# Kernel optimization log

Hardware: AMD Instinct MI355X
Metric: run time of the kernel (lower is better)

## Reference

```python
import jax, jax.numpy as jnp
import numpy as np

GROUPS = 32
EPS = 1e-5
N_HEADS = 4


def group_norm(x, w, b):
    # x: [B, C, T]; GroupNorm over (C/G, T) within each of G groups
    B, C, T = x.shape
    xg = x.reshape(B, GROUPS, (C // GROUPS) * T)
    mean = xg.mean(axis=-1, keepdims=True)
    var = xg.var(axis=-1, keepdims=True)
    xn = ((xg - mean) * jax.lax.rsqrt(var + EPS)).reshape(B, C, T)
    return xn * w[None, :, None] + b[None, :, None]


def setup_inputs() -> dict:
    key = jax.random.key(0)
    ks = jax.random.split(key, 5)
    B, C, H, W = 2, 256, 64, 64
    x = jax.random.normal(ks[0], (B, C, H, W), dtype=jnp.float32)
    norm_w = jnp.ones((C,), dtype=jnp.float32)
    norm_b = jnp.zeros((C,), dtype=jnp.float32)
    qkv_w = jax.random.normal(ks[1], (3 * C, C), dtype=jnp.float32) * (C ** -0.5)
    qkv_b = jax.random.normal(ks[2], (3 * C,), dtype=jnp.float32) * 0.02
    proj_w = jax.random.normal(ks[3], (C, C), dtype=jnp.float32) * (C ** -0.5)
    proj_b = jax.random.normal(ks[4], (C,), dtype=jnp.float32) * 0.02
    return {"x": x, "norm_w": norm_w, "norm_b": norm_b,
            "qkv_w": qkv_w, "qkv_b": qkv_b,
            "proj_w": proj_w, "proj_b": proj_b}


def reference(x, norm_w, norm_b, qkv_w, qkv_b, proj_w, proj_b):
    B, C, Hs, Ws = x.shape
    T = Hs * Ws
    xf = x.reshape(B, C, T)
    xn = group_norm(xf, norm_w, norm_b)
    # 1x1 conv1d == channel matmul: [3C,C] x [B,C,T] -> [B,3C,T]
    qkv = jnp.einsum('oc,bct->bot', qkv_w, xn) + qkv_b[None, :, None]
    ch = C // N_HEADS
    # legacy order: [B, H*3*ch, T] -> [B*H, 3*ch, T] -> split
    qkv_h = qkv.reshape(B * N_HEADS, 3 * ch, T)
    q, k, v = qkv_h[:, :ch], qkv_h[:, ch:2 * ch], qkv_h[:, 2 * ch:]
    scale = ch ** -0.25
    # full [B*H, T, T] score matrix, softmax in fp32 (faithful to source)
    weight = jnp.einsum('bct,bcs->bts', q * scale, k * scale)
    weight = jax.nn.softmax(weight.astype(jnp.float32), axis=-1).astype(qkv.dtype)
    a = jnp.einsum('bts,bcs->bct', weight, v).reshape(B, C, T)
    h = jnp.einsum('oc,bct->bot', proj_w, a) + proj_b[None, :, None]
    return (xf + h).reshape(B, C, Hs, Ws)
```

## Files before the change

### kernel.cpp

```cpp
#include <hip/hip_runtime.h>
#include <hip/hip_bf16.h>

#define B_    2
#define C_    256
#define T_    4096
#define GRP   32
#define CPG   8
#define NH    4
#define CH    64
#define K3C   768
#define SPLIT 4
#define GSL   8
#define NSTAT (B_ * GRP * GSL)
#define NCVT  128
#define LOG2E 1.4426950408889634f

typedef __attribute__((ext_vector_type(8))) short bf16x8;
typedef __attribute__((ext_vector_type(4))) float f32x4;
typedef __attribute__((ext_vector_type(16))) float f32x16;

#if __has_builtin(__builtin_amdgcn_exp2f)
#define EXP2(x) __builtin_amdgcn_exp2f(x)
#else
#define EXP2(x) exp2f(x)
#endif

__device__ __forceinline__ unsigned pk2(float a, float b) {
    __hip_bfloat162 h = __float22bfloat162_rn(make_float2(a, b));
    union { __hip_bfloat162 h2; unsigned u; } cv; cv.h2 = h;
    return cv.u;
}
__device__ __forceinline__ float bf2f(unsigned short u) {
    return __uint_as_float((unsigned)u << 16);
}

__device__ __forceinline__ void gl_lds16(const unsigned short* g, unsigned short* l) {
    __builtin_amdgcn_global_load_lds(
        (const __attribute__((address_space(1))) unsigned int*)g,
        (__attribute__((address_space(3))) unsigned int*)l,
        16, 0, 0);
}


__global__ __launch_bounds__(256) void pre_kernel(
    const float* __restrict__ x, float* __restrict__ stat,
    const float* __restrict__ qw, const float* __restrict__ pw,
    unsigned short* __restrict__ qwb, unsigned short* __restrict__ pwb) {
    int bid = blockIdx.x;
    int tid = threadIdx.x;
    if (bid < NSTAT) {
        int bg = bid >> 3, sl = bid & 7;
        const int SLN = CPG * T_ / GSL;
        const float* xp = x + (size_t)bg * CPG * T_ + (size_t)sl * SLN;
        float s = 0.f, s2 = 0.f;
        for (int i = tid * 4; i < SLN; i += 1024) {
            float4 v = *(const float4*)&xp[i];
            s  += (v.x + v.y) + (v.z + v.w);
            s2 += (v.x * v.x + v.y * v.y) + (v.z * v.z + v.w * v.w);
        }
        for (int off = 32; off > 0; off >>= 1) {
            s  += __shfl_down(s,  off);
            s2 += __shfl_down(s2, off);
        }
        __shared__ float rs[4], rs2[4];
        int wid = tid >> 6;
        if ((tid & 63) == 0) { rs[wid] = s; rs2[wid] = s2; }
        __syncthreads();
        if (tid == 0) {
            stat[bid * 2]     = (rs[0] + rs[1]) + (rs[2] + rs[3]);
            stat[bid * 2 + 1] = (rs2[0] + rs2[1]) + (rs2[2] + rs2[3]);
        }
    } else {
        int i = (bid - NSTAT) * 256 + tid;
        const int n1 = K3C * C_ / 8;
        const float* src; unsigned short* dst;
        if (i < n1) { src = qw + 8 * i; dst = qwb + 8 * i; }
        else { int j = i - n1; src = pw + 8 * j; dst = pwb + 8 * j; }
        float4 a = *(const float4*)src;
        float4 b = *(const float4*)(src + 4);
        uint4 u;
        u.x = pk2(a.x, a.y); u.y = pk2(a.z, a.w);
        u.z = pk2(b.x, b.y); u.w = pk2(b.z, b.w);
        *(uint4*)dst = u;
    }
}

__global__ __launch_bounds__(256) void gn_apply_kernel(
    const float* __restrict__ x, const float* __restrict__ stat,
    const float* __restrict__ w, const float* __restrict__ b,
    unsigned short* __restrict__ xnT) {
    int bg = blockIdx.x, sl = blockIdx.y;
    int batch = bg / GRP, g = bg % GRP;
    const float* xp = x + (size_t)bg * CPG * T_;
    int tid = threadIdx.x;

    float s = 0.f, s2 = 0.f;
#pragma unroll
    for (int i = 0; i < GSL; ++i) {
        s  += stat[(bg * GSL + i) * 2];
        s2 += stat[(bg * GSL + i) * 2 + 1];
    }
    float inv_n = 1.f / (float)(CPG * T_);
    float mean = s * inv_n;
    float var  = s2 * inv_n - mean * mean;
    float inv  = rsqrtf(var + 1e-5f);

    float wv[8], bv[8];
#pragma unroll
    for (int j = 0; j < 8; j++) {
        float ww = w[g * CPG + j] * inv;
        wv[j] = ww;
        bv[j] = b[g * CPG + j] - mean * ww;
    }
    int t0 = sl * (T_ / GSL);
#pragma unroll
    for (int rep = 0; rep < 2; ++rep) {
        int t = t0 + rep * 256 + tid;
        float v[8];
#pragma unroll
        for (int j = 0; j < 8; j++) v[j] = xp[(size_t)j * T_ + t] * wv[j] + bv[j];
        uint4 u;
        u.x = pk2(v[0], v[1]); u.y = pk2(v[2], v[3]);
        u.z = pk2(v[4], v[5]); u.w = pk2(v[6], v[7]);
        *(uint4*)&xnT[(((size_t)batch * 256 + (t >> 4)) * 32 + g) * 128
                      + (t & 15) * 8] = u;
    }
}

__global__ __launch_bounds__(256) void qkv_gemm_kernel(
    const unsigned short* __restrict__ Wb, const float* __restrict__ bias,
    const unsigned short* __restrict__ Xt, unsigned short* __restrict__ q_t,
    unsigned short* __restrict__ k_t, unsigned short* __restrict__ v_d) {
    int tb = blockIdx.x * 128;
    int by = blockIdx.y;
    int bz = blockIdx.z;
    int ob = by * 64;
    int tid = threadIdx.x;
    int l = tid & 15, oct = (tid >> 4) & 3, w = tid >> 6;

    __shared__ __align__(16) unsigned short SH[64 * 264];

#pragma unroll
    for (int j = 0; j < 8; ++j) {
        int idx = tid + 256 * j;
        int row = idx >> 5, ch = idx & 31;
        *(uint4*)&SH[row * 264 + ch * 8] =
            *(const uint4*)&Wb[(size_t)(ob + row) * C_ + ch * 8];
    }
    __syncthreads();

    f32x4 acc[4][2];
#pragma unroll
    for (int mf = 0; mf < 4; ++mf)
#pragma unroll
        for (int nf = 0; nf < 2; ++nf) acc[mf][nf] = (f32x4){0.f, 0.f, 0.f, 0.f};

#pragma unroll
    for (int kk = 0; kk < 8; ++kk) {
        int c0 = 32 * kk + 8 * oct;
        bf16x8 bfr[2];
#pragma unroll
        for (int nf = 0; nf < 2; ++nf)
            bfr[nf] = *(const bf16x8*)
                &Xt[(((size_t)bz * 256 + (tb >> 4) + 2 * w + nf) * 32
                     + 4 * kk + oct) * 128 + l * 8];
#pragma unroll
        for (int mf = 0; mf < 4; ++mf) {
            bf16x8 af = *(const bf16x8*)&SH[(16 * mf + l) * 264 + c0];
#pragma unroll
            for (int nf = 0; nf < 2; ++nf)
                acc[mf][nf] = __builtin_amdgcn_mfma_f32_16x16x32_bf16(af, bfr[nf], acc[mf][nf], 0, 0, 0);
        }
    }

    int head = by / 3, sec = by - 3 * head;
    int bh = bz * NH + head;

    if (sec < 2) {
        float scale = (sec == 0) ? 0.125f * LOG2E : 1.f;
        unsigned short* dst = ((sec == 0) ? q_t : k_t) + (size_t)bh * T_ * CH;
#pragma unroll
        for (int mf = 0; mf < 4; ++mf) {
            float bvs[4];
#pragma unroll
            for (int r = 0; r < 4; ++r) bvs[r] = bias[ob + 16 * mf + 4 * oct + r];
#pragma unroll
            for (int nf = 0; nf < 2; ++nf) {
                int t = tb + 32 * w + 16 * nf + l;
                float v0 = (acc[mf][nf][0] + bvs[0]) * scale;
                float v1 = (acc[mf][nf][1] + bvs[1]) * scale;
                float v2 = (acc[mf][nf][2] + bvs[2]) * scale;
                float v3 = (acc[mf][nf][3] + bvs[3]) * scale;
                uint2 u; u.x = pk2(v0, v1); u.y = pk2(v2, v3);
                *(uint2*)&dst[(size_t)t * CH + 16 * mf + 4 * oct] = u;
            }
        }
    } else {
        __syncthreads();
#pragma unroll
        for (int mf = 0; mf < 4; ++mf) {
            float bvs[4];
#pragma unroll
            for (int r = 0; r < 4; ++r) bvs[r] = bias[ob + 16 * mf + 4 * oct + r];
#pragma unroll
            for (int nf = 0; nf < 2; ++nf) {
                int tl = 32 * w + 16 * nf + l;
#pragma unroll
                for (int r = 0; r < 4; ++r) {
                    unsigned pv = pk2(acc[mf][nf][r] + bvs[r], 0.f);
                    SH[(16 * mf + 4 * oct + r) * 136 + tl] = (unsigned short)(pv & 0xffffu);
                }
            }
        }
        __syncthreads();
        unsigned short* vdst = v_d + (size_t)bh * CH * T_;
#pragma unroll
        for (int j = 0; j < 4; ++j) {
            int idx = tid + 256 * j;
            int row = idx >> 4, ch = idx & 15;
            *(uint4*)&vdst[(size_t)row * T_ + tb + ch * 8] =
                *(uint4*)&SH[row * 136 + ch * 8];
        }
    }
}

__global__ __launch_bounds__(256, 4) void attn_kernel(
    const unsigned short* __restrict__ q_t, const unsigned short* __restrict__ k_t,
    const unsigned short* __restrict__ v_d, unsigned short* __restrict__ Opart,
    float* __restrict__ lbuf) {
    int bh = blockIdx.y;
    int sp = blockIdx.z;
    int t0 = blockIdx.x * 128;
    int tid = threadIdx.x;
    int ln = tid & 63;
    int li = ln & 31;
    int hi = ln >> 5;
    int w  = tid >> 6;
    int l7 = li & 7;
    int sw = l7 ^ ((li >> 3) & 3);

    __shared__ __align__(16) unsigned short Kt[2][64 * 64];
    __shared__ __align__(16) unsigned short Vt[2][64 * 64];

    const unsigned short* qb = q_t + (size_t)bh * T_ * CH;
    const unsigned short* kb = k_t + (size_t)bh * T_ * CH;
    const unsigned short* vb = v_d + (size_t)bh * CH * T_;

    int tq = t0 + 32 * w + li;
    bf16x8 qf[4];
#pragma unroll
    for (int ks = 0; ks < 4; ++ks)
        qf[ks] = *(const bf16x8*)&qb[(size_t)tq * CH + ks * 16 + 8 * hi];

    int rsub = ln >> 3;
    int sch  = ln & 7;
    int cm8_0 = (sch ^ rsub ^ ((2 * w) & 3)) * 8;
    int cm8_1 = (sch ^ rsub ^ ((2 * w + 1) & 3)) * 8;
    int kr0 = 16 * w + rsub;

#define STAGE(buf, s0) do {                                                            \
    gl_lds16(kb + (size_t)((s0) + kr0) * CH + cm8_0,     &Kt[buf][(16 * w) * 64]);     \
    gl_lds16(kb + (size_t)((s0) + kr0 + 8) * CH + cm8_1, &Kt[buf][(16 * w + 8) * 64]); \
    gl_lds16(vb + (size_t)kr0 * T_ + (s0) + cm8_0,       &Vt[buf][(16 * w) * 64]);     \
    gl_lds16(vb + (size_t)(kr0 + 8) * T_ + (s0) + cm8_1, &Vt[buf][(16 * w + 8) * 64]); \
} while (0)

    f32x16 O0, O1;
#pragma unroll
    for (int i = 0; i < 16; ++i) { O0[i] = 0.f; O1[i] = 0.f; }
    float l_run = 0.f;

    int s_beg = sp * (T_ / SPLIT);
    const int NT = (T_ / SPLIT) / 64;

    STAGE(0, s_beg);
    __syncthreads();

    int cur = 0;
    for (int t = 0; t < NT; ++t) {
        if (t + 1 < NT) STAGE(cur ^ 1, s_beg + (t + 1) * 64);

        f32x16 S0, S1;
#pragma unroll
        for (int i = 0; i < 16; ++i) { S0[i] = 0.f; S1[i] = 0.f; }
        __builtin_amdgcn_s_setprio(1);
#pragma unroll
        for (int ks = 0; ks < 4; ++ks) {
            bf16x8 ka0 = *(const bf16x8*)
                &Kt[cur][li * 64 + (((2 * ks + hi) ^ sw) * 8)];
            bf16x8 ka1 = *(const bf16x8*)
                &Kt[cur][(32 + li) * 64 + (((2 * ks + hi) ^ sw) * 8)];
            S0 = __builtin_amdgcn_mfma_f32_32x32x16_bf16(ka0, qf[ks], S0, 0, 0, 0);
            S1 = __builtin_amdgcn_mfma_f32_32x32x16_bf16(ka1, qf[ks], S1, 0, 0, 0);
        }
        __builtin_amdgcn_s_setprio(0);

        unsigned W0[8], W1[8];
        float lloc = 0.f;
#pragma unroll
        for (int h = 0; h < 4; ++h) {
            float a0 = EXP2(S0[4 * h + 0]), a1 = EXP2(S0[4 * h + 1]);
            float a2 = EXP2(S0[4 * h + 2]), a3 = EXP2(S0[4 * h + 3]);
            float b0 = EXP2(S1[4 * h + 0]), b1 = EXP2(S1[4 * h + 1]);
            float b2 = EXP2(S1[4 * h + 2]), b3 = EXP2(S1[4 * h + 3]);
            lloc += ((a0 + a1) + (a2 + a3)) + ((b0 + b1) + (b2 + b3));
            W0[2 * h] = pk2(a0, a1); W0[2 * h + 1] = pk2(a2, a3);
            W1[2 * h] = pk2(b0, b1); W1[2 * h + 1] = pk2(b2, b3);
        }
        l_run += lloc;

        __builtin_amdgcn_s_setprio(1);
#pragma unroll
        for (int g = 0; g < 4; ++g) {
            int ks = g & 1;
            unsigned w0, w1, w2, w3;
            if (g < 2) {
                w0 = W0[4 * ks + 0]; w1 = W0[4 * ks + 1];
                w2 = W0[4 * ks + 2]; w3 = W0[4 * ks + 3];
            } else {
                w0 = W1[4 * ks + 0]; w1 = W1[4 * ks + 1];
                w2 = W1[4 * ks + 2]; w3 = W1[4 * ks + 3];
            }
            asm("v_permlane32_swap_b32 %0, %1" : "+v"(w0), "+v"(w2));
            asm("v_permlane32_swap_b32 %0, %1" : "+v"(w1), "+v"(w3));
            union { unsigned u[4]; bf16x8 v; } pu;
            pu.u[0] = w0; pu.u[1] = w1; pu.u[2] = w2; pu.u[3] = w3;
            bf16x8 va0 = *(const bf16x8*)
                &Vt[cur][li * 64 + (((2 * g + hi) ^ sw) * 8)];
            bf16x8 va1 = *(const bf16x8*)
                &Vt[cur][(32 + li) * 64 + (((2 * g + hi) ^ sw) * 8)];
            O0 = __builtin_amdgcn_mfma_f32_32x32x16_bf16(va0, pu.v, O0, 0, 0, 0);
            O1 = __builtin_amdgcn_mfma_f32_32x32x16_bf16(va1, pu.v, O1, 0, 0, 0);
        }
        __builtin_amdgcn_s_setprio(0);

        __syncthreads();
        cur ^= 1;
    }
#undef STAGE

    float lt = l_run + __shfl_xor(l_run, 32);
    float inv = 1.f / lt;
    size_t obase = ((size_t)(sp * 8 + bh) * 256 + (tq >> 4)) * 8;
    int ti = tq & 15;
#pragma unroll
    for (int cb = 0; cb < 2; ++cb) {
#pragma unroll
        for (int h = 0; h < 4; ++h) {
            float v0, v1, v2, v3;
            if (cb == 0) {
                v0 = O0[4 * h + 0]; v1 = O0[4 * h + 1];
                v2 = O0[4 * h + 2]; v3 = O0[4 * h + 3];
            } else {
                v0 = O1[4 * h + 0]; v1 = O1[4 * h + 1];
                v2 = O1[4 * h + 2]; v3 = O1[4 * h + 3];
            }
            uint2 u;
            u.x = pk2(v0 * inv, v1 * inv);
            u.y = pk2(v2 * inv, v3 * inv);
            *(uint2*)&Opart[(obase + 4 * cb + h) * 128 + ti * 8 + 4 * hi] = u;
        }
    }
    if (hi == 0) lbuf[(size_t)(sp * 8 + bh) * T_ + tq] = lt;
}

__global__ __launch_bounds__(256) void proj_gemm_kernel(
    const unsigned short* __restrict__ Wb, const float* __restrict__ bias,
    const unsigned short* __restrict__ Opart, const float* __restrict__ lbuf,
    const float* __restrict__ xres, float* __restrict__ out) {
    int tb = blockIdx.x * 64;
    int ob = blockIdx.y * 64;
    int bz = blockIdx.z;
    int tid = threadIdx.x;
    int l = tid & 15, oct = (tid >> 4) & 3, w = tid >> 6;

    __shared__ __align__(16) unsigned short SH[64 * 264];

#pragma unroll
    for (int j = 0; j < 8; ++j) {
        int idx = tid + 256 * j;
        int row = idx >> 5, ch = idx & 31;
        *(uint4*)&SH[row * 264 + ch * 8] =
            *(const uint4*)&Wb[(size_t)(ob + row) * C_ + ch * 8];
    }
    __syncthreads();

    int t = tb + 16 * w + l;

    float lwn[SPLIT][NH];
#pragma unroll
    for (int h = 0; h < NH; ++h) {
        float lw[SPLIT], lsum = 0.f;
#pragma unroll
        for (int sp = 0; sp < SPLIT; ++sp) {
            lw[sp] = lbuf[(size_t)(sp * 8 + bz * NH + h) * T_ + t];
            lsum += lw[sp];
        }
        float inv = 1.f / lsum;
#pragma unroll
        for (int sp = 0; sp < SPLIT; ++sp) lwn[sp][h] = lw[sp] * inv;
    }

    f32x4 acc[4];
#pragma unroll
    for (int mf = 0; mf < 4; ++mf) acc[mf] = (f32x4){0.f, 0.f, 0.f, 0.f};

#pragma unroll
    for (int kk = 0; kk < 8; ++kk) {
        int c0 = 32 * kk + 8 * oct;
        int h  = kk >> 1;
        int cc = 4 * (kk & 1) + oct;

        float o[8];
#pragma unroll
        for (int j = 0; j < 8; ++j) o[j] = 0.f;
#pragma unroll
        for (int sp = 0; sp < SPLIT; ++sp) {
            const unsigned short* p = Opart +
                (((size_t)(sp * 8 + bz * NH + h) * 256 + (t >> 4)) * 8 + cc) * 128
                + (t & 15) * 8;
            uint4 u = *(const uint4*)p;
            float s = lwn[sp][h];
            o[0] += bf2f((unsigned short)(u.x & 0xffffu)) * s;
            o[1] += bf2f((unsigned short)(u.x >> 16)) * s;
            o[2] += bf2f((unsigned short)(u.y & 0xffffu)) * s;
            o[3] += bf2f((unsigned short)(u.y >> 16)) * s;
            o[4] += bf2f((unsigned short)(u.z & 0xffffu)) * s;
            o[5] += bf2f((unsigned short)(u.z >> 16)) * s;
            o[6] += bf2f((unsigned short)(u.w & 0xffffu)) * s;
            o[7] += bf2f((unsigned short)(u.w >> 16)) * s;
        }
        union { uint4 u; bf16x8 v; } pb;
        pb.u.x = pk2(o[0], o[1]); pb.u.y = pk2(o[2], o[3]);
        pb.u.z = pk2(o[4], o[5]); pb.u.w = pk2(o[6], o[7]);

#pragma unroll
        for (int mf = 0; mf < 4; ++mf) {
            bf16x8 af = *(const bf16x8*)&SH[(16 * mf + l) * 264 + c0];
            acc[mf] = __builtin_amdgcn_mfma_f32_16x16x32_bf16(af, pb.v, acc[mf], 0, 0, 0);
        }
    }

#pragma unroll
    for (int mf = 0; mf < 4; ++mf) {
#pragma unroll
        for (int r = 0; r < 4; ++r) {
            int o = ob + 16 * mf + 4 * oct + r;
            size_t idx = ((size_t)bz * C_ + o) * T_ + t;
            out[idx] = acc[mf][r] + bias[o] + xres[idx];
        }
    }
}

extern "C" void kernel_launch(void* const* d_in, const int* in_sizes, int n_in,
                              void* d_out, int out_size, void* d_ws, size_t ws_size,
                              hipStream_t stream) {
    const float* x      = (const float*)d_in[0];
    const float* norm_w = (const float*)d_in[1];
    const float* norm_b = (const float*)d_in[2];
    const float* qkv_w  = (const float*)d_in[3];
    const float* qkv_b  = (const float*)d_in[4];
    const float* proj_w = (const float*)d_in[5];
    const float* proj_b = (const float*)d_in[6];
    float* out = (float*)d_out;

    char* p = (char*)d_ws;
    unsigned short* xnT = (unsigned short*)p; p += (size_t)B_ * T_ * C_ * 2;
    unsigned short* qwb = (unsigned short*)p; p += (size_t)K3C * C_ * 2;
    unsigned short* pwb = (unsigned short*)p; p += (size_t)C_ * C_ * 2;
    unsigned short* q_t = (unsigned short*)p; p += (size_t)B_ * NH * T_ * CH * 2;
    unsigned short* k_t = (unsigned short*)p; p += (size_t)B_ * NH * T_ * CH * 2;
    unsigned short* v_d = (unsigned short*)p; p += (size_t)B_ * NH * T_ * CH * 2;
    unsigned short* Opart = (unsigned short*)p; p += (size_t)SPLIT * 8 * T_ * CH * 2;
    float* lbuf         = (float*)p;          p += (size_t)SPLIT * 8 * T_ * 4;
    float* stat         = (float*)p;          p += (size_t)NSTAT * 2 * 4;

    pre_kernel<<<dim3(NSTAT + NCVT), dim3(256), 0, stream>>>(
        x, stat, qkv_w, proj_w, qwb, pwb);
    gn_apply_kernel<<<dim3(B_ * GRP, GSL), dim3(256), 0, stream>>>(
        x, stat, norm_w, norm_b, xnT);
    qkv_gemm_kernel<<<dim3(T_ / 128, 12, B_), dim3(256), 0, stream>>>(
        qwb, qkv_b, xnT, q_t, k_t, v_d);
    attn_kernel<<<dim3(T_ / 128, B_ * NH, SPLIT), dim3(256), 0, stream>>>(
        q_t, k_t, v_d, Opart, lbuf);
    proj_gemm_kernel<<<dim3(T_ / 64, C_ / 64, B_), dim3(256), 0, stream>>>(
        pwb, proj_b, Opart, lbuf, x, out);
}
```

Baseline: 135.5 us.

## Raise attention occupancy with single-buffered LDS, split-8 and XCD-aware block mapping

The attention kernel now splits the key range into 8 chunks instead of 4 and launches as a flat 1D grid. Block IDs are remapped so each XCD works on contiguous head/split slices, which should improve L2 locality. LDS double buffering is dropped for a single buffer per K and V, and the launch bound asks for 8 blocks per CU, so latency is hidden by more resident waves instead of prefetching. Smaller changes precompute LDS read pointers and start the first MFMA from a zero vector rather than zeroing the accumulators each tile. The costs are a sync-exposed load on every tile, tighter register limits, and twice as many partial outputs for the projection kernel to reduce.

```diff
diff --git a/kernel.cpp b/kernel.cpp
--- a/kernel.cpp
+++ b/kernel.cpp
@@ -9,7 +9,7 @@
 #define NH    4
 #define CH    64
 #define K3C   768
-#define SPLIT 4
+#define SPLIT 8
 #define GSL   8
 #define NSTAT (B_ * GRP * GSL)
 #define NCVT  128
@@ -224,13 +224,19 @@
     }
 }
 
-__global__ __launch_bounds__(256, 4) void attn_kernel(
+__global__ __launch_bounds__(256, 8) void attn_kernel(
     const unsigned short* __restrict__ q_t, const unsigned short* __restrict__ k_t,
     const unsigned short* __restrict__ v_d, unsigned short* __restrict__ Opart,
     float* __restrict__ lbuf) {
-    int bh = blockIdx.y;
-    int sp = blockIdx.z;
-    int t0 = blockIdx.x * 128;
+    int id = blockIdx.x;
+    int xcd = id & 7;
+    int j = id >> 3;
+    int slice = xcd * 8 + (j >> 5);
+    int bx = j & 31;
+    int bh = slice >> 3;
+    int sp = slice & 7;
+    int t0 = bx * 128;
+
     int tid = threadIdx.x;
     int ln = tid & 63;
     int li = ln & 31;
@@ -239,8 +245,8 @@
     int l7 = li & 7;
     int sw = l7 ^ ((li >> 3) & 3);
 
-    __shared__ __align__(16) unsigned short Kt[2][64 * 64];
-    __shared__ __align__(16) unsigned short Vt[2][64 * 64];
+    __shared__ __align__(16) unsigned short Kt[64 * 64];
+    __shared__ __align__(16) unsigned short Vt[64 * 64];
 
     const unsigned short* qb = q_t + (size_t)bh * T_ * CH;
     const unsigned short* kb = k_t + (size_t)bh * T_ * CH;
@@ -251,6 +257,15 @@
 #pragma unroll
     for (int ks = 0; ks < 4; ++ks)
         qf[ks] = *(const bf16x8*)&qb[(size_t)tq * CH + ks * 16 + 8 * hi];
+
+    const unsigned short* kbp[4];
+    const unsigned short* vbp[4];
+#pragma unroll
+    for (int ks = 0; ks < 4; ++ks) {
+        int co = ((2 * ks + hi) ^ sw) * 8;
+        kbp[ks] = &Kt[li * 64 + co];
+        vbp[ks] = &Vt[li * 64 + co];
+    }
 
     int rsub = ln >> 3;
     int sch  = ln & 7;
@@ -258,38 +273,37 @@
     int cm8_1 = (sch ^ rsub ^ ((2 * w + 1) & 3)) * 8;
     int kr0 = 16 * w + rsub;
 
-#define STAGE(buf, s0) do {                                                            \
-    gl_lds16(kb + (size_t)((s0) + kr0) * CH + cm8_0,     &Kt[buf][(16 * w) * 64]);     \
-    gl_lds16(kb + (size_t)((s0) + kr0 + 8) * CH + cm8_1, &Kt[buf][(16 * w + 8) * 64]); \
-    gl_lds16(vb + (size_t)kr0 * T_ + (s0) + cm8_0,       &Vt[buf][(16 * w) * 64]);     \
-    gl_lds16(vb + (size_t)(kr0 + 8) * T_ + (s0) + cm8_1, &Vt[buf][(16 * w + 8) * 64]); \
+#define STAGE(s0) do {                                                            \
+    gl_lds16(kb + (size_t)((s0) + kr0) * CH + cm8_0,     &Kt[(16 * w) * 64]);     \
+    gl_lds16(kb + (size_t)((s0) + kr0 + 8) * CH + cm8_1, &Kt[(16 * w + 8) * 64]); \
+    gl_lds16(vb + (size_t)kr0 * T_ + (s0) + cm8_0,       &Vt[(16 * w) * 64]);     \
+    gl_lds16(vb + (size_t)(kr0 + 8) * T_ + (s0) + cm8_1, &Vt[(16 * w + 8) * 64]); \
 } while (0)
 
-    f32x16 O0, O1;
-#pragma unroll
-    for (int i = 0; i < 16; ++i) { O0[i] = 0.f; O1[i] = 0.f; }
+    f32x16 O0, O1, Zv;
+#pragma unroll
+    for (int i = 0; i < 16; ++i) { O0[i] = 0.f; O1[i] = 0.f; Zv[i] = 0.f; }
     float l_run = 0.f;
 
     int s_beg = sp * (T_ / SPLIT);
     const int NT = (T_ / SPLIT) / 64;
 
-    STAGE(0, s_beg);
-    __syncthreads();
-
-    int cur = 0;
     for (int t = 0; t < NT; ++t) {
-        if (t + 1 < NT) STAGE(cur ^ 1, s_beg + (t + 1) * 64);
+        STAGE(s_beg + t * 64);
+        __syncthreads();
 
         f32x16 S0, S1;
-#pragma unroll
-        for (int i = 0; i < 16; ++i) { S0[i] = 0.f; S1[i] = 0.f; }
         __builtin_amdgcn_s_setprio(1);
-#pragma unroll
-        for (int ks = 0; ks < 4; ++ks) {
-            bf16x8 ka0 = *(const bf16x8*)
-                &Kt[cur][li * 64 + (((2 * ks + hi) ^ sw) * 8)];
-            bf16x8 ka1 = *(const bf16x8*)
-                &Kt[cur][(32 + li) * 64 + (((2 * ks + hi) ^ sw) * 8)];
+        {
+            bf16x8 ka0 = *(const bf16x8*)(kbp[0]);
+            bf16x8 ka1 = *(const bf16x8*)(kbp[0] + 2048);
+            S0 = __builtin_amdgcn_mfma_f32_32x32x16_bf16(ka0, qf[0], Zv, 0, 0, 0);
+            S1 = __builtin_amdgcn_mfma_f32_32x32x16_bf16(ka1, qf[0], Zv, 0, 0, 0);
+        }
+#pragma unroll
+        for (int ks = 1; ks < 4; ++ks) {
+            bf16x8 ka0 = *(const bf16x8*)(kbp[ks]);
+            bf16x8 ka1 = *(const bf16x8*)(kbp[ks] + 2048);
             S0 = __builtin_amdgcn_mfma_f32_32x32x16_bf16(ka0, qf[ks], S0, 0, 0, 0);
             S1 = __builtin_amdgcn_mfma_f32_32x32x16_bf16(ka1, qf[ks], S1, 0, 0, 0);
         }
@@ -325,17 +339,14 @@
             asm("v_permlane32_swap_b32 %0, %1" : "+v"(w1), "+v"(w3));
             union { unsigned u[4]; bf16x8 v; } pu;
             pu.u[0] = w0; pu.u[1] = w1; pu.u[2] = w2; pu.u[3] = w3;
-            bf16x8 va0 = *(const bf16x8*)
-                &Vt[cur][li * 64 + (((2 * g + hi) ^ sw) * 8)];
-            bf16x8 va1 = *(const bf16x8*)
-                &Vt[cur][(32 + li) * 64 + (((2 * g + hi) ^ sw) * 8)];
+            bf16x8 va0 = *(const bf16x8*)(vbp[g]);
+            bf16x8 va1 = *(const bf16x8*)(vbp[g] + 2048);
             O0 = __builtin_amdgcn_mfma_f32_32x32x16_bf16(va0, pu.v, O0, 0, 0, 0);
             O1 = __builtin_amdgcn_mfma_f32_32x32x16_bf16(va1, pu.v, O1, 0, 0, 0);
         }
         __builtin_amdgcn_s_setprio(0);
 
         __syncthreads();
-        cur ^= 1;
     }
 #undef STAGE
 
@@ -481,7 +492,7 @@
         x, stat, norm_w, norm_b, xnT);
     qkv_gemm_kernel<<<dim3(T_ / 128, 12, B_), dim3(256), 0, stream>>>(
         qwb, qkv_b, xnT, q_t, k_t, v_d);
-    attn_kernel<<<dim3(T_ / 128, B_ * NH, SPLIT), dim3(256), 0, stream>>>(
+    attn_kernel<<<dim3(T_ / 128 * B_ * NH * SPLIT), dim3(256), 0, stream>>>(
         q_t, k_t, v_d, Opart, lbuf);
     proj_gemm_kernel<<<dim3(T_ / 64, C_ / 64, B_), dim3(256), 0, stream>>>(
         pwb, proj_b, Opart, lbuf, x, out);
```

After: 443.1 us. +226.9%, slower.
